# Optimization experiments

Measured on AMD Instinct MI355X. Metric: run time of the kernel, lower is better.

## Reference

```python
import jax, jax.numpy as jnp
import numpy as np

EPS_NORM = 1e-4
EPS_LOG = 1e-6


def normed_weight(W):
    # W: [O, I, K] (K=1). normalize() over dims (1,2) per output channel,
    # with norm scaled by alpha = sqrt(O / (O*I*K)) = 1/sqrt(I*K), then
    # divided again by sqrt(I*K) in get_normed_weight (eval path).
    O, I, K = W.shape
    fan_in = I * K
    norm = jnp.sqrt(jnp.sum(jnp.square(W), axis=(1, 2), keepdims=True))  # [O,1,1]
    norm = EPS_NORM + norm / np.sqrt(fan_in)
    return (W / norm) / np.sqrt(fan_in)


def complex_log(x):
    real = jnp.log(jnp.maximum(jnp.abs(x), EPS_LOG))
    imag = jnp.where(x < 0, jnp.pi, 0.0).astype(real.dtype)
    return jax.lax.complex(real, imag)


def logcumsumexp_complex(z, axis=-1):
    # stable complex logcumsumexp via associative scan:
    # logaddexp(a, b) = m + log(exp(a-m) + exp(b-m)), m = max(Re a, Re b)
    def combine(a, b):
        m = jnp.maximum(a.real, b.real)
        mc = jax.lax.complex(m, jnp.zeros_like(m))
        return mc + jnp.log(jnp.exp(a - mc) + jnp.exp(b - mc))
    return jax.lax.associative_scan(combine, z, axis=axis)


def min_gru(h, g):
    # h, g: [B, C, L]; parallel log-space minGRU recurrence along L
    log_scale = 0.5 * jnp.log(1.0 / jnp.cosh(g) + 1.0)
    log_coeffs = -jax.nn.softplus(g) + log_scale                 # real
    log_values = (-jax.nn.softplus(-g) + log_scale) + complex_log(h)  # complex
    a_star = jnp.cumsum(log_coeffs, axis=-1)                     # real
    a_star_c = jax.lax.complex(a_star, jnp.zeros_like(a_star))
    log_h = a_star_c + logcumsumexp_complex(log_values - a_star_c, axis=-1)
    return jnp.exp(log_h).real


def scaled_cat(xs, axis):
    Ns = [x.shape[axis] for x in xs]
    scale = np.sqrt(np.mean(Ns))
    return scale * jnp.concatenate([x * n ** -0.5 for n, x in zip(Ns, xs)], axis=axis)


def setup_inputs() -> dict:
    key = jax.random.key(0)
    k1, k2 = jax.random.split(key)
    B, D, L = 8, 512, 8192
    x = jax.random.normal(k1, (B, D, L), dtype=jnp.float32)
    W = jax.random.normal(k2, (2 * D, D, 1), dtype=jnp.float32)  # Conv1d(dim, 2*dim, 1) weight
    return {"x": x, "W": W}


def reference(x, W):
    Wn = normed_weight(W)  # [2D, D, 1]
    fb = jnp.einsum('oi,bil->bol', Wn[:, :, 0], x)  # [B, 2D, L]
    fore, back = jnp.split(fb, 2, axis=1)
    h_f, g_f = jnp.split(fore, 2, axis=1)
    back_r = back[..., ::-1]
    h_b, g_b = jnp.split(back_r, 2, axis=1)
    out_f = min_gru(h_f, g_f)
    out_b = min_gru(h_b, g_b)[..., ::-1]
    return scaled_cat([out_f, out_b], axis=1)
```

## Files before the change

### kernel.cpp

```cpp
#include <hip/hip_runtime.h>
#include <math.h>
#include <stdint.h>

#define LSEQ 8192
#define DIN  512
#define NB   8
#define NO   1024

typedef __bf16 bf16x8 __attribute__((ext_vector_type(8)));
typedef float f32x16 __attribute__((ext_vector_type(16)));

__device__ __forceinline__ uint32_t pack_bf16_rne(float lo, float hi) {
    uint32_t ul = __builtin_bit_cast(uint32_t, lo);
    uint32_t uh = __builtin_bit_cast(uint32_t, hi);
    ul += 0x7FFFu + ((ul >> 16) & 1u);
    uh += 0x7FFFu + ((uh >> 16) & 1u);
    return (ul >> 16) | (uh & 0xFFFF0000u);
}

__global__ void norm_kernel(const float* __restrict__ W, uint32_t* __restrict__ Wnb) {
    const int o = blockIdx.x;
    const int lane = threadIdx.x;
    const float* row = W + (size_t)o * DIN;
    float4 v0 = *(const float4*)(row + lane * 4);
    float4 v1 = *(const float4*)(row + 256 + lane * 4);
    float s = v0.x * v0.x + v0.y * v0.y + v0.z * v0.z + v0.w * v0.w
            + v1.x * v1.x + v1.y * v1.y + v1.z * v1.z + v1.w * v1.w;
#pragma unroll
    for (int m = 32; m; m >>= 1) s += __shfl_xor(s, m, 64);
    const float sq = 22.62741699796952f;
    const float scale = 1.0f / ((1e-4f + sqrtf(s) / sq) * sq);
    uint2 w0, w1;
    w0.x = pack_bf16_rne(v0.x * scale, v0.y * scale);
    w0.y = pack_bf16_rne(v0.z * scale, v0.w * scale);
    w1.x = pack_bf16_rne(v1.x * scale, v1.y * scale);
    w1.y = pack_bf16_rne(v1.z * scale, v1.w * scale);
    *(uint2*)&Wnb[o * 256 + lane * 2] = w0;
    *(uint2*)&Wnb[o * 256 + 128 + lane * 2] = w1;
}

__global__ __launch_bounds__(256)
void gemm_kernel(const uint16_t* __restrict__ Wnb, const float* __restrict__ x,
                 float* __restrict__ out, float* __restrict__ g_buf) {
    __shared__ uint32_t sA[2048];
    __shared__ uint32_t sB[16 * 132];

    const int tid  = threadIdx.x;
    const int lane = tid & 63;
    const int w    = tid >> 6;
    const int wm   = w & 1, wn = w >> 1;

    const int o0 = blockIdx.x * 128;
    const int l0 = blockIdx.y * 128;
    const int b  = blockIdx.z;

    const float* xb = x + (size_t)b * DIN * LSEQ + l0;

    const int am = tid >> 1;
    const int aq = (tid & 1) * 2;
    const uint16_t* arow = Wnb + (size_t)(o0 + am) * DIN + aq * 8;
    const uint32_t aw0 = am * 16 + ((aq ^ (am & 3)) * 4);
    const uint32_t aw1 = am * 16 + (((aq + 1) ^ (am & 3)) * 4);

    const int k2a = tid >> 5, lqa = tid & 31;
    const int k2b = (tid + 256) >> 5, lqb = tid & 31;

    f32x16 acc[2][2];
#pragma unroll
    for (int i = 0; i < 2; ++i)
#pragma unroll
        for (int j = 0; j < 2; ++j)
#pragma unroll
            for (int r = 0; r < 16; ++r) acc[i][j][r] = 0.f;

    uint4 aR0, aR1;
    float4 bR0, bR1, bR2, bR3;
    {
        aR0 = *(const uint4*)(arow);
        aR1 = *(const uint4*)(arow + 8);
        const float* p0 = xb + (size_t)(2 * k2a) * LSEQ + lqa * 4;
        bR0 = *(const float4*)(p0);
        bR1 = *(const float4*)(p0 + LSEQ);
        const float* p1 = xb + (size_t)(2 * k2b) * LSEQ + lqb * 4;
        bR2 = *(const float4*)(p1);
        bR3 = *(const float4*)(p1 + LSEQ);
    }

#pragma unroll 1
    for (int it = 0; it < 16; ++it) {
        __syncthreads();
        *(uint4*)&sA[aw0] = aR0;
        *(uint4*)&sA[aw1] = aR1;
        {
            uint4 w0, w1;
            w0.x = pack_bf16_rne(bR0.x, bR1.x);
            w0.y = pack_bf16_rne(bR0.y, bR1.y);
            w0.z = pack_bf16_rne(bR0.z, bR1.z);
            w0.w = pack_bf16_rne(bR0.w, bR1.w);
            *(uint4*)&sB[k2a * 132 + lqa * 4] = w0;
            w1.x = pack_bf16_rne(bR2.x, bR3.x);
            w1.y = pack_bf16_rne(bR2.y, bR3.y);
            w1.z = pack_bf16_rne(bR2.z, bR3.z);
            w1.w = pack_bf16_rne(bR2.w, bR3.w);
            *(uint4*)&sB[k2b * 132 + lqb * 4] = w1;
        }
        __syncthreads();
        if (it + 1 < 16) {
            const int kt = (it + 1) * 32;
            aR0 = *(const uint4*)(arow + kt);
            aR1 = *(const uint4*)(arow + kt + 8);
            const float* p0 = xb + (size_t)(kt + 2 * k2a) * LSEQ + lqa * 4;
            bR0 = *(const float4*)(p0);
            bR1 = *(const float4*)(p0 + LSEQ);
            const float* p1 = xb + (size_t)(kt + 2 * k2b) * LSEQ + lqb * 4;
            bR2 = *(const float4*)(p1);
            bR3 = *(const float4*)(p1 + LSEQ);
        }
#pragma unroll
        for (int kh = 0; kh < 2; ++kh) {
            bf16x8 af[2], bfr[2];
#pragma unroll
            for (int ms = 0; ms < 2; ++ms) {
                const int m = wm * 64 + ms * 32 + (lane & 31);
                const int q = kh * 2 + (lane >> 5);
                af[ms] = *(const bf16x8*)&sA[m * 16 + ((q ^ (m & 3)) * 4)];
            }
#pragma unroll
            for (int ns = 0; ns < 2; ++ns) {
                const int col = wn * 64 + ns * 32 + (lane & 31);
                const int rb = kh * 8 + (lane >> 5) * 4;
                uint4 t;
                t.x = sB[(rb + 0) * 132 + col];
                t.y = sB[(rb + 1) * 132 + col];
                t.z = sB[(rb + 2) * 132 + col];
                t.w = sB[(rb + 3) * 132 + col];
                bfr[ns] = __builtin_bit_cast(bf16x8, t);
            }
#pragma unroll
            for (int ms = 0; ms < 2; ++ms)
#pragma unroll
                for (int ns = 0; ns < 2; ++ns)
                    acc[ms][ns] = __builtin_amdgcn_mfma_f32_32x32x16_bf16(
                        af[ms], bfr[ns], acc[ms][ns], 0, 0, 0);
        }
    }

    const int sec = o0 >> 8;
    float* dst = (sec & 1) ? g_buf : out;
    const int row0 = (sec >> 1) * 256 + (o0 & 255);
    float* base = dst + (size_t)b * 512 * LSEQ + l0;
#pragma unroll
    for (int ms = 0; ms < 2; ++ms)
#pragma unroll
        for (int ns = 0; ns < 2; ++ns) {
            const f32x16 a = acc[ms][ns];
            const int rb = row0 + wm * 64 + ms * 32 + 4 * (lane >> 5);
            const int cc = wn * 64 + ns * 32 + (lane & 31);
#pragma unroll
            for (int r = 0; r < 16; ++r) {
                const int row = rb + (r & 3) + 8 * (r >> 2);
                base[(size_t)row * LSEQ + cc] = a[r];
            }
        }
}

__global__ __launch_bounds__(256)
void scan_kernel(const float* __restrict__ g_buf, float* __restrict__ out) {
    __shared__ float sbuf[4][2048];
    __shared__ float sAc[4], sBc[4];

    const int r = blockIdx.x;
    const int b = blockIdx.y;
    const int dir = r >> 8;
    const int t = threadIdx.x;
    const int lane = t & 63;
    const int w = t >> 6;

    const size_t rowoff = ((size_t)b * 512 + r) * LSEQ;
    const float* hrow = out + rowoff;
    const float* grow = g_buf + rowoff;
    float* orow = out + rowoff;

    float* sw = sbuf[w];
    const int wbase = w * 2048;

#pragma unroll
    for (int i = 0; i < 8; ++i) {
        float4 v = *(const float4*)(hrow + wbase + i * 256 + lane * 4);
        const uint32_t g = i * 64 + lane;
        const uint32_t gs = g ^ ((g >> 3) & 7);
        *(float4*)&sw[gs * 4] = v;
    }
    asm volatile("s_waitcnt lgkmcnt(0)" ::: "memory");
    float hv[32];
#pragma unroll
    for (int q = 0; q < 8; ++q) {
        const uint32_t g = lane * 8 + q;
        const uint32_t gs = g ^ ((g >> 3) & 7);
        float4 v = *(const float4*)&sw[gs * 4];
        hv[q * 4 + 0] = v.x; hv[q * 4 + 1] = v.y;
        hv[q * 4 + 2] = v.z; hv[q * 4 + 3] = v.w;
    }
#pragma unroll
    for (int i = 0; i < 8; ++i) {
        float4 v = *(const float4*)(grow + wbase + i * 256 + lane * 4);
        const uint32_t g = i * 64 + lane;
        const uint32_t gs = g ^ ((g >> 3) & 7);
        *(float4*)&sw[gs * 4] = v;
    }
    asm volatile("s_waitcnt lgkmcnt(0)" ::: "memory");
    float av[32], vv[32];
#pragma unroll
    for (int q = 0; q < 8; ++q) {
        const uint32_t g = lane * 8 + q;
        const uint32_t gs = g ^ ((g >> 3) & 7);
        float4 gq = *(const float4*)&sw[gs * 4];
        float gsv[4] = {gq.x, gq.y, gq.z, gq.w};
#pragma unroll
        for (int s = 0; s < 4; ++s) {
            const int mo = q * 4 + s;
            float g_ = fminf(fmaxf(gsv[s], -30.f), 30.f);
            float eg = __expf(g_);
            float a  = rsqrtf(fmaf(eg, eg, 1.f));
            float c  = a * eg;
            float h_ = hv[mo];
            av[mo] = a;
            vv[mo] = c * copysignf(fmaxf(fabsf(h_), 1e-6f), h_);
        }
    }

    float A = 1.f, B = 0.f;
    if (dir == 0) {
#pragma unroll
        for (int i = 0; i < 32; ++i) { B = fmaf(av[i], B, vv[i]); A *= av[i]; }
    } else {
#pragma unroll
        for (int i = 31; i >= 0; --i) { B = fmaf(av[i], B, vv[i]); A *= av[i]; }
    }
    if (dir == 0) {
#pragma unroll
        for (int off = 1; off < 64; off <<= 1) {
            float Ap = __shfl_up(A, (unsigned)off, 64);
            float Bp = __shfl_up(B, (unsigned)off, 64);
            if (lane >= off) { B = fmaf(A, Bp, B); A *= Ap; }
        }
        if (lane == 63) { sAc[w] = A; sBc[w] = B; }
    } else {
#pragma unroll
        for (int off = 1; off < 64; off <<= 1) {
            float Ap = __shfl_down(A, (unsigned)off, 64);
            float Bp = __shfl_down(B, (unsigned)off, 64);
            if (lane + off < 64) { B = fmaf(A, Bp, B); A *= Ap; }
        }
        if (lane == 0) { sAc[w] = A; sBc[w] = B; }
    }
    __syncthreads();
    float WB = 0.f;
    if (dir == 0) { for (int wv = 0; wv < w; ++wv) WB = fmaf(sAc[wv], WB, sBc[wv]); }
    else          { for (int wv = 3; wv > w; --wv) WB = fmaf(sAc[wv], WB, sBc[wv]); }
    float eA, eB;
    if (dir == 0) {
        eA = __shfl_up(A, 1u, 64); eB = __shfl_up(B, 1u, 64);
        if (lane == 0) { eA = 1.f; eB = 0.f; }
    } else {
        eA = __shfl_down(A, 1u, 64); eB = __shfl_down(B, 1u, 64);
        if (lane == 63) { eA = 1.f; eB = 0.f; }
    }
    float H = fmaf(eA, WB, eB);

    if (dir == 0) {
#pragma unroll
        for (int i = 0; i < 32; ++i) { H = fmaf(av[i], H, vv[i]); vv[i] = H; }
    } else {
#pragma unroll
        for (int i = 31; i >= 0; --i) { H = fmaf(av[i], H, vv[i]); vv[i] = H; }
    }

#pragma unroll
    for (int q = 0; q < 8; ++q) {
        const uint32_t g = lane * 8 + q;
        const uint32_t gs = g ^ ((g >> 3) & 7);
        *(float4*)&sw[gs * 4] = make_float4(vv[q * 4], vv[q * 4 + 1], vv[q * 4 + 2], vv[q * 4 + 3]);
    }
    asm volatile("s_waitcnt lgkmcnt(0)" ::: "memory");
#pragma unroll
    for (int i = 0; i < 8; ++i) {
        const uint32_t g = i * 64 + lane;
        const uint32_t gs = g ^ ((g >> 3) & 7);
        float4 v = *(const float4*)&sw[gs * 4];
        *(float4*)(orow + wbase + i * 256 + lane * 4) = v;
    }
}

extern "C" void kernel_launch(void* const* d_in, const int* in_sizes, int n_in,
                              void* d_out, int out_size, void* d_ws, size_t ws_size,
                              hipStream_t stream) {
    const float* x = (const float*)d_in[0];
    const float* W = (const float*)d_in[1];
    float* out = (float*)d_out;

    uint32_t* Wnb  = (uint32_t*)d_ws;
    float*    g_buf = (float*)((char*)d_ws + (size_t)NO * DIN * 2);

    norm_kernel<<<dim3(NO), dim3(64), 0, stream>>>(W, Wnb);
    gemm_kernel<<<dim3(8, 64, NB), dim3(256), 0, stream>>>(
        (const uint16_t*)Wnb, x, out, g_buf);
    scan_kernel<<<dim3(512, NB), dim3(256), 0, stream>>>(g_buf, out);
}
```

Measured before the change: 430.9 us.

## Store GEMM intermediate as packed bf16 pairs and scan two channels per block

The GEMM now writes its output as bf16, packing two adjacent output channels per 32-bit word into one workspace buffer. This replaces the separate fp32 h and g buffers and roughly halves intermediate write and read traffic. The scan kernel uses 512 threads and processes a pair of channels per block, reading packed h and g words and writing two fp32 output rows. The GEMM grid is also remapped so consecutive blocks are grouped by XCD for better L2 locality. Rounding h and g to bf16 adds precision loss before the exponential recurrence.

```diff
diff --git a/kernel.cpp b/kernel.cpp
--- a/kernel.cpp
+++ b/kernel.cpp
@@ -16,6 +16,12 @@
     ul += 0x7FFFu + ((ul >> 16) & 1u);
     uh += 0x7FFFu + ((uh >> 16) & 1u);
     return (ul >> 16) | (uh & 0xFFFF0000u);
+}
+__device__ __forceinline__ float bf16_lo(uint32_t w) {
+    return __builtin_bit_cast(float, w << 16);
+}
+__device__ __forceinline__ float bf16_hi(uint32_t w) {
+    return __builtin_bit_cast(float, w & 0xFFFF0000u);
 }
 
 __global__ void norm_kernel(const float* __restrict__ W, uint32_t* __restrict__ Wnb) {
@@ -41,7 +47,7 @@
 
 __global__ __launch_bounds__(256)
 void gemm_kernel(const uint16_t* __restrict__ Wnb, const float* __restrict__ x,
-                 float* __restrict__ out, float* __restrict__ g_buf) {
+                 uint32_t* __restrict__ fbp) {
     __shared__ uint32_t sA[2048];
     __shared__ uint32_t sB[16 * 132];
 
@@ -50,9 +56,12 @@
     const int w    = tid >> 6;
     const int wm   = w & 1, wn = w >> 1;
 
-    const int o0 = blockIdx.x * 128;
-    const int l0 = blockIdx.y * 128;
-    const int b  = blockIdx.z;
+    const int bx  = blockIdx.x;
+    const int xcd = bx & 7;
+    const int t   = bx >> 3;
+    const int o0  = (t & 7) * 128;
+    const int l0  = (xcd + ((t >> 3) << 3)) * 128;
+    const int b   = blockIdx.y;
 
     const float* xb = x + (size_t)b * DIN * LSEQ + l0;
 
@@ -129,12 +138,12 @@
             for (int ns = 0; ns < 2; ++ns) {
                 const int col = wn * 64 + ns * 32 + (lane & 31);
                 const int rb = kh * 8 + (lane >> 5) * 4;
-                uint4 t;
-                t.x = sB[(rb + 0) * 132 + col];
-                t.y = sB[(rb + 1) * 132 + col];
-                t.z = sB[(rb + 2) * 132 + col];
-                t.w = sB[(rb + 3) * 132 + col];
-                bfr[ns] = __builtin_bit_cast(bf16x8, t);
+                uint4 tt;
+                tt.x = sB[(rb + 0) * 132 + col];
+                tt.y = sB[(rb + 1) * 132 + col];
+                tt.z = sB[(rb + 2) * 132 + col];
+                tt.w = sB[(rb + 3) * 132 + col];
+                bfr[ns] = __builtin_bit_cast(bf16x8, tt);
             }
 #pragma unroll
             for (int ms = 0; ms < 2; ++ms)
@@ -145,150 +154,188 @@
         }
     }
 
-    const int sec = o0 >> 8;
-    float* dst = (sec & 1) ? g_buf : out;
-    const int row0 = (sec >> 1) * 256 + (o0 & 255);
-    float* base = dst + (size_t)b * 512 * LSEQ + l0;
+    uint32_t* fbp_b = fbp + (size_t)b * 512 * LSEQ + l0;
 #pragma unroll
     for (int ms = 0; ms < 2; ++ms)
 #pragma unroll
         for (int ns = 0; ns < 2; ++ns) {
             const f32x16 a = acc[ms][ns];
-            const int rb = row0 + wm * 64 + ms * 32 + 4 * (lane >> 5);
+            const int rb = o0 + wm * 64 + ms * 32 + 4 * (lane >> 5);
             const int cc = wn * 64 + ns * 32 + (lane & 31);
 #pragma unroll
-            for (int r = 0; r < 16; ++r) {
+            for (int rp = 0; rp < 8; ++rp) {
+                const int r = rp * 2;
                 const int row = rb + (r & 3) + 8 * (r >> 2);
-                base[(size_t)row * LSEQ + cc] = a[r];
-            }
-        }
-}
-
-__global__ __launch_bounds__(256)
-void scan_kernel(const float* __restrict__ g_buf, float* __restrict__ out) {
-    __shared__ float sbuf[4][2048];
-    __shared__ float sAc[4], sBc[4];
-
-    const int r = blockIdx.x;
-    const int b = blockIdx.y;
-    const int dir = r >> 8;
-    const int t = threadIdx.x;
+                fbp_b[(size_t)(row >> 1) * LSEQ + cc] = pack_bf16_rne(a[r], a[r + 1]);
+            }
+        }
+}
+
+__global__ __launch_bounds__(512)
+void scan_kernel(const uint32_t* __restrict__ fbp, float* __restrict__ out) {
+    __shared__ uint32_t sbuf[8][2048];
+    __shared__ float sA0[8], sB0[8], sA1[8], sB1[8];
+
+    const int bx  = blockIdx.x;
+    const int b   = blockIdx.y;
+    const int dir = bx >> 7;
+    const int p   = bx & 127;
+    const int o2h = dir * 256 + p;
+    const int o2g = dir * 256 + 128 + p;
+
+    const int t    = threadIdx.x;
     const int lane = t & 63;
-    const int w = t >> 6;
-
-    const size_t rowoff = ((size_t)b * 512 + r) * LSEQ;
-    const float* hrow = out + rowoff;
-    const float* grow = g_buf + rowoff;
-    float* orow = out + rowoff;
-
-    float* sw = sbuf[w];
-    const int wbase = w * 2048;
-
-#pragma unroll
-    for (int i = 0; i < 8; ++i) {
-        float4 v = *(const float4*)(hrow + wbase + i * 256 + lane * 4);
+    const int w    = t >> 6;
+
+    const uint32_t* hwp = fbp + ((size_t)b * 512 + o2h) * LSEQ + w * 1024;
+    const uint32_t* gwp = fbp + ((size_t)b * 512 + o2g) * LSEQ + w * 1024;
+    uint32_t* sw = sbuf[w];
+    float* swf = (float*)sbuf[w];
+
+#pragma unroll
+    for (int i = 0; i < 4; ++i) {
+        uint4 v = *(const uint4*)(hwp + i * 256 + lane * 4);
         const uint32_t g = i * 64 + lane;
         const uint32_t gs = g ^ ((g >> 3) & 7);
-        *(float4*)&sw[gs * 4] = v;
+        *(uint4*)&sw[gs * 4] = v;
+    }
+#pragma unroll
+    for (int i = 0; i < 4; ++i) {
+        uint4 v = *(const uint4*)(gwp + i * 256 + lane * 4);
+        const uint32_t g = i * 64 + lane;
+        const uint32_t gs = g ^ ((g >> 3) & 7);
+        *(uint4*)&sw[1024 + gs * 4] = v;
     }
     asm volatile("s_waitcnt lgkmcnt(0)" ::: "memory");
-    float hv[32];
-#pragma unroll
-    for (int q = 0; q < 8; ++q) {
-        const uint32_t g = lane * 8 + q;
-        const uint32_t gs = g ^ ((g >> 3) & 7);
-        float4 v = *(const float4*)&sw[gs * 4];
-        hv[q * 4 + 0] = v.x; hv[q * 4 + 1] = v.y;
-        hv[q * 4 + 2] = v.z; hv[q * 4 + 3] = v.w;
-    }
-#pragma unroll
-    for (int i = 0; i < 8; ++i) {
-        float4 v = *(const float4*)(grow + wbase + i * 256 + lane * 4);
-        const uint32_t g = i * 64 + lane;
-        const uint32_t gs = g ^ ((g >> 3) & 7);
-        *(float4*)&sw[gs * 4] = v;
-    }
-    asm volatile("s_waitcnt lgkmcnt(0)" ::: "memory");
-    float av[32], vv[32];
-#pragma unroll
-    for (int q = 0; q < 8; ++q) {
-        const uint32_t g = lane * 8 + q;
-        const uint32_t gs = g ^ ((g >> 3) & 7);
-        float4 gq = *(const float4*)&sw[gs * 4];
-        float gsv[4] = {gq.x, gq.y, gq.z, gq.w};
+
+    float av0[16], vv0[16], av1[16], vv1[16];
+#pragma unroll
+    for (int q = 0; q < 4; ++q) {
+        const uint32_t g = lane * 4 + q;
+        const uint32_t gs = g ^ ((g >> 3) & 7);
+        uint4 hw4 = *(const uint4*)&sw[gs * 4];
+        uint4 gw4 = *(const uint4*)&sw[1024 + gs * 4];
+        const uint32_t hws[4] = {hw4.x, hw4.y, hw4.z, hw4.w};
+        const uint32_t gws[4] = {gw4.x, gw4.y, gw4.z, gw4.w};
 #pragma unroll
         for (int s = 0; s < 4; ++s) {
             const int mo = q * 4 + s;
-            float g_ = fminf(fmaxf(gsv[s], -30.f), 30.f);
-            float eg = __expf(g_);
-            float a  = rsqrtf(fmaf(eg, eg, 1.f));
-            float c  = a * eg;
-            float h_ = hv[mo];
-            av[mo] = a;
-            vv[mo] = c * copysignf(fmaxf(fabsf(h_), 1e-6f), h_);
-        }
-    }
-
-    float A = 1.f, B = 0.f;
-    if (dir == 0) {
-#pragma unroll
-        for (int i = 0; i < 32; ++i) { B = fmaf(av[i], B, vv[i]); A *= av[i]; }
-    } else {
-#pragma unroll
-        for (int i = 31; i >= 0; --i) { B = fmaf(av[i], B, vv[i]); A *= av[i]; }
-    }
+            {
+                float g_ = fminf(fmaxf(bf16_lo(gws[s]), -30.f), 30.f);
+                float eg = __expf(g_);
+                float a  = rsqrtf(fmaf(eg, eg, 1.f));
+                float h_ = bf16_lo(hws[s]);
+                av0[mo] = a;
+                vv0[mo] = a * eg * copysignf(fmaxf(fabsf(h_), 1e-6f), h_);
+            }
+            {
+                float g_ = fminf(fmaxf(bf16_hi(gws[s]), -30.f), 30.f);
+                float eg = __expf(g_);
+                float a  = rsqrtf(fmaf(eg, eg, 1.f));
+                float h_ = bf16_hi(hws[s]);
+                av1[mo] = a;
+                vv1[mo] = a * eg * copysignf(fmaxf(fabsf(h_), 1e-6f), h_);
+            }
+        }
+    }
+
+    float A0 = 1.f, B0 = 0.f, A1 = 1.f, B1 = 0.f;
+    if (dir == 0) {
+#pragma unroll
+        for (int i = 0; i < 16; ++i) {
+            B0 = fmaf(av0[i], B0, vv0[i]); A0 *= av0[i];
+            B1 = fmaf(av1[i], B1, vv1[i]); A1 *= av1[i];
+        }
+    } else {
+#pragma unroll
+        for (int i = 15; i >= 0; --i) {
+            B0 = fmaf(av0[i], B0, vv0[i]); A0 *= av0[i];
+            B1 = fmaf(av1[i], B1, vv1[i]); A1 *= av1[i];
+        }
+    }
+
     if (dir == 0) {
 #pragma unroll
         for (int off = 1; off < 64; off <<= 1) {
-            float Ap = __shfl_up(A, (unsigned)off, 64);
-            float Bp = __shfl_up(B, (unsigned)off, 64);
-            if (lane >= off) { B = fmaf(A, Bp, B); A *= Ap; }
-        }
-        if (lane == 63) { sAc[w] = A; sBc[w] = B; }
+            float Ap0 = __shfl_up(A0, (unsigned)off, 64), Bp0 = __shfl_up(B0, (unsigned)off, 64);
+            float Ap1 = __shfl_up(A1, (unsigned)off, 64), Bp1 = __shfl_up(B1, (unsigned)off, 64);
+            if (lane >= off) {
+                B0 = fmaf(A0, Bp0, B0); A0 *= Ap0;
+                B1 = fmaf(A1, Bp1, B1); A1 *= Ap1;
+            }
+        }
+        if (lane == 63) { sA0[w] = A0; sB0[w] = B0; sA1[w] = A1; sB1[w] = B1; }
     } else {
 #pragma unroll
         for (int off = 1; off < 64; off <<= 1) {
-            float Ap = __shfl_down(A, (unsigned)off, 64);
-            float Bp = __shfl_down(B, (unsigned)off, 64);
-            if (lane + off < 64) { B = fmaf(A, Bp, B); A *= Ap; }
-        }
-        if (lane == 0) { sAc[w] = A; sBc[w] = B; }
+            float Ap0 = __shfl_down(A0, (unsigned)off, 64), Bp0 = __shfl_down(B0, (unsigned)off, 64);
+            float Ap1 = __shfl_down(A1, (unsigned)off, 64), Bp1 = __shfl_down(B1, (unsigned)off, 64);
+            if (lane + off < 64) {
+                B0 = fmaf(A0, Bp0, B0); A0 *= Ap0;
+                B1 = fmaf(A1, Bp1, B1); A1 *= Ap1;
+            }
+        }
+        if (lane == 0) { sA0[w] = A0; sB0[w] = B0; sA1[w] = A1; sB1[w] = B1; }
     }
     __syncthreads();
-    float WB = 0.f;
-    if (dir == 0) { for (int wv = 0; wv < w; ++wv) WB = fmaf(sAc[wv], WB, sBc[wv]); }
-    else          { for (int wv = 3; wv > w; --wv) WB = fmaf(sAc[wv], WB, sBc[wv]); }
-    float eA, eB;
-    if (dir == 0) {
-        eA = __shfl_up(A, 1u, 64); eB = __shfl_up(B, 1u, 64);
-        if (lane == 0) { eA = 1.f; eB = 0.f; }
-    } else {
-        eA = __shfl_down(A, 1u, 64); eB = __shfl_down(B, 1u, 64);
-        if (lane == 63) { eA = 1.f; eB = 0.f; }
-    }
-    float H = fmaf(eA, WB, eB);
-
-    if (dir == 0) {
-#pragma unroll
-        for (int i = 0; i < 32; ++i) { H = fmaf(av[i], H, vv[i]); vv[i] = H; }
-    } else {
-#pragma unroll
-        for (int i = 31; i >= 0; --i) { H = fmaf(av[i], H, vv[i]); vv[i] = H; }
-    }
-
-#pragma unroll
-    for (int q = 0; q < 8; ++q) {
-        const uint32_t g = lane * 8 + q;
-        const uint32_t gs = g ^ ((g >> 3) & 7);
-        *(float4*)&sw[gs * 4] = make_float4(vv[q * 4], vv[q * 4 + 1], vv[q * 4 + 2], vv[q * 4 + 3]);
+    float WB0 = 0.f, WB1 = 0.f;
+    if (dir == 0) {
+        for (int wv = 0; wv < w; ++wv) {
+            WB0 = fmaf(sA0[wv], WB0, sB0[wv]);
+            WB1 = fmaf(sA1[wv], WB1, sB1[wv]);
+        }
+    } else {
+        for (int wv = 7; wv > w; --wv) {
+            WB0 = fmaf(sA0[wv], WB0, sB0[wv]);
+            WB1 = fmaf(sA1[wv], WB1, sB1[wv]);
+        }
+    }
+    float eA0, eB0, eA1, eB1;
+    if (dir == 0) {
+        eA0 = __shfl_up(A0, 1u, 64); eB0 = __shfl_up(B0, 1u, 64);
+        eA1 = __shfl_up(A1, 1u, 64); eB1 = __shfl_up(B1, 1u, 64);
+        if (lane == 0) { eA0 = 1.f; eB0 = 0.f; eA1 = 1.f; eB1 = 0.f; }
+    } else {
+        eA0 = __shfl_down(A0, 1u, 64); eB0 = __shfl_down(B0, 1u, 64);
+        eA1 = __shfl_down(A1, 1u, 64); eB1 = __shfl_down(B1, 1u, 64);
+        if (lane == 63) { eA0 = 1.f; eB0 = 0.f; eA1 = 1.f; eB1 = 0.f; }
+    }
+    float H0 = fmaf(eA0, WB0, eB0);
+    float H1 = fmaf(eA1, WB1, eB1);
+
+    if (dir == 0) {
+#pragma unroll
+        for (int i = 0; i < 16; ++i) {
+            H0 = fmaf(av0[i], H0, vv0[i]); vv0[i] = H0;
+            H1 = fmaf(av1[i], H1, vv1[i]); vv1[i] = H1;
+        }
+    } else {
+#pragma unroll
+        for (int i = 15; i >= 0; --i) {
+            H0 = fmaf(av0[i], H0, vv0[i]); vv0[i] = H0;
+            H1 = fmaf(av1[i], H1, vv1[i]); vv1[i] = H1;
+        }
+    }
+
+#pragma unroll
+    for (int q = 0; q < 4; ++q) {
+        const uint32_t g = lane * 4 + q;
+        const uint32_t gs = g ^ ((g >> 3) & 7);
+        *(float4*)&swf[gs * 4] =
+            make_float4(vv0[q * 4], vv0[q * 4 + 1], vv0[q * 4 + 2], vv0[q * 4 + 3]);
+        *(float4*)&swf[1024 + gs * 4] =
+            make_float4(vv1[q * 4], vv1[q * 4 + 1], vv1[q * 4 + 2], vv1[q * 4 + 3]);
     }
     asm volatile("s_waitcnt lgkmcnt(0)" ::: "memory");
-#pragma unroll
-    for (int i = 0; i < 8; ++i) {
+    const int c0 = 2 * p, c1 = 2 * p + 1;
+    float* orow0 = out + ((size_t)b * 512 + dir * 256 + c0) * LSEQ + w * 1024;
+    float* orow1 = out + ((size_t)b * 512 + dir * 256 + c1) * LSEQ + w * 1024;
+#pragma unroll
+    for (int i = 0; i < 4; ++i) {
         const uint32_t g = i * 64 + lane;
         const uint32_t gs = g ^ ((g >> 3) & 7);
-        float4 v = *(const float4*)&sw[gs * 4];
-        *(float4*)(orow + wbase + i * 256 + lane * 4) = v;
+        *(float4*)(orow0 + i * 256 + lane * 4) = *(const float4*)&swf[gs * 4];
+        *(float4*)(orow1 + i * 256 + lane * 4) = *(const float4*)&swf[1024 + gs * 4];
     }
 }
 
@@ -299,11 +346,10 @@
     const float* W = (const float*)d_in[1];
     float* out = (float*)d_out;
 
-    uint32_t* Wnb  = (uint32_t*)d_ws;
-    float*    g_buf = (float*)((char*)d_ws + (size_t)NO * DIN * 2);
+    uint32_t* Wnb = (uint32_t*)d_ws;
+    uint32_t* fbp = (uint32_t*)((char*)d_ws + (size_t)NO * DIN * 2);
 
     norm_kernel<<<dim3(NO), dim3(64), 0, stream>>>(W, Wnb);
-    gemm_kernel<<<dim3(8, 64, NB), dim3(256), 0, stream>>>(
-        (const uint16_t*)Wnb, x, out, g_buf);
-    scan_kernel<<<dim3(512, NB), dim3(256), 0, stream>>>(g_buf, out);
-}
+    gemm_kernel<<<dim3(512, NB), dim3(256), 0, stream>>>((const uint16_t*)Wnb, x, fbp);
+    scan_kernel<<<dim3(256, NB), dim3(512), 0, stream>>>(fbp, out);
+}
```

New measurement: 357.2 us. 1.21x faster.
